# Performance work log

Measured on AMD Instinct MI355X. Metric: run time of the kernel, lower is better.

## Reference

```python
import jax, jax.numpy as jnp
import numpy as np

# dims: batch, nodes, d_node, d_edge, d_attn_hid, heads, d_node_hid, d_edge_hid, layers
B, N, DN, DE, DH, H, DNH, DEH, L = 2, 256, 128, 64, 128, 8, 512, 256, 2
DHH = DH // H  # per-head dim
SCALE = 1.0 / (DH ** 0.5)  # source scales by full d_hid, not per-head dim


def _ln(x, g, b):
    m = jnp.mean(x, -1, keepdims=True)
    v = jnp.mean((x - m) ** 2, -1, keepdims=True)
    return (x - m) * jax.lax.rsqrt(v + 1e-5) * g + b


def _gelu(x):
    return jax.nn.gelu(x, approximate=False)  # torch nn.GELU default = exact erf


def setup_inputs() -> dict:
    key = jax.random.key(0)
    ks = iter(jax.random.split(key, 40))
    def w(shape, scale=0.02):
        return jax.random.normal(next(ks), shape, jnp.float32) * scale
    return {
        "node_features": jax.random.normal(next(ks), (B, N, DN), jnp.float32),
        "edge_features": jax.random.normal(next(ks), (B, N, N, DE), jnp.float32),
        "Wqkv_n": w((L, DN, 3 * DH)),
        "Wqkv_e": w((L, DE, 4 * DH)),
        "Wo": w((L, DH, DN)), "bo": jnp.zeros((L, DN), jnp.float32),
        "Wl0": w((L, DN, DN)), "bl0": jnp.zeros((L, DN), jnp.float32),
        "ln0_g": jnp.ones((L, DN), jnp.float32), "ln0_b": jnp.zeros((L, DN), jnp.float32),
        "Wm1": w((L, DN, DNH)), "Wm2": w((L, DNH, DN)), "bm2": jnp.zeros((L, DN), jnp.float32),
        "ln1_g": jnp.ones((L, DN), jnp.float32), "ln1_b": jnp.zeros((L, DN), jnp.float32),
        "We0": w((L, 2 * DE, DEH)), "be0": jnp.zeros((L, DEH), jnp.float32),
        "Ws": w((L, DN, DEH)), "bs": jnp.zeros((L, DEH), jnp.float32),
        "Wt": w((L, DN, DEH)), "bt": jnp.zeros((L, DEH), jnp.float32),
        "We1": w((L, DEH, DE)), "be1": jnp.zeros((L, DE), jnp.float32),
        "eln0_g": jnp.ones((L, DE), jnp.float32), "eln0_b": jnp.zeros((L, DE), jnp.float32),
        "Wem1": w((L, DE, DEH)), "Wem2": w((L, DEH, DE)), "bem2": jnp.zeros((L, DE), jnp.float32),
        "eln1_g": jnp.ones((L, DE), jnp.float32), "eln1_b": jnp.zeros((L, DE), jnp.float32),
    }


def _forward(node_features, edge_features, Wqkv_n, Wqkv_e, Wo, bo, Wl0, bl0,
             ln0_g, ln0_b, Wm1, Wm2, bm2, ln1_g, ln1_b, We0, be0, Ws, bs, Wt, bt,
             We1, be1, eln0_g, eln0_b, Wem1, Wem2, bem2, eln1_g, eln1_b):
    x, e = node_features, edge_features
    for l in range(L):
        # --- RTAttention (modulate_v=True, eval mode) ---
        qkv_n = (x @ Wqkv_n[l]).reshape(B, N, H, 3 * DHH).transpose(0, 2, 1, 3)  # b h n 3d
        qn, kn, vn = jnp.split(qkv_n, 3, axis=-1)
        qkv_e = (e @ Wqkv_e[l]).reshape(B, N, N, H, 4 * DHH).transpose(0, 3, 1, 2, 4)  # b h i j 4d
        eq, ek, ev, em = jnp.split(qkv_e, 4, axis=-1)
        q = qn[:, :, :, None, :] + eq            # b h i j d
        k = kn[:, :, None, :, :] + ek            # b h i j d
        v = vn[:, :, None, :, :] * em + ev       # modulated values
        dots = SCALE * jnp.einsum('bhijd,bhijd->bhij', q, k)
        attn = jax.nn.softmax(dots, axis=-1)
        out = jnp.einsum('bhij,bhijd->bhid', attn, v)
        out = out.transpose(0, 2, 1, 3).reshape(B, N, DH)
        attn_out = out @ Wo[l] + bo[l]
        # --- node updates: ln(x + lin0(attn)); ln(x + mlp(x)) ---
        x = _ln(x + (attn_out @ Wl0[l] + bl0[l]), ln0_g[l], ln0_b[l])
        x = _ln(x + (_gelu(x @ Wm1[l]) @ Wm2[l] + bm2[l]), ln1_g[l], ln1_b[l])
        # --- edge updates (EdgeLayer) ---
        src = (x @ Ws[l] + bs[l])[:, :, None, :]   # broadcast over target j
        tgt = (x @ Wt[l] + bt[l])[:, None, :, :]   # broadcast over source i
        ecat = jnp.concatenate([e, e.transpose(0, 2, 1, 3)], axis=-1)  # [e_ij, e_ji]
        h = _gelu(ecat @ We0[l] + be0[l] + src + tgt)
        e = _ln(e + (h @ We1[l] + be1[l]), eln0_g[l], eln0_b[l])
        e = _ln(e + (_gelu(e @ Wem1[l]) @ Wem2[l] + bem2[l]), eln1_g[l], eln1_b[l])
    return x, e


def reference(node_features, edge_features, Wqkv_n, Wqkv_e, Wo, bo, Wl0, bl0,
              ln0_g, ln0_b, Wm1, Wm2, bm2, ln1_g, ln1_b, We0, be0, Ws, bs, Wt, bt,
              We1, be1, eln0_g, eln0_b, Wem1, Wem2, bem2, eln1_g, eln1_b):
    return _forward(node_features, edge_features, Wqkv_n, Wqkv_e, Wo, bo, Wl0, bl0,
                    ln0_g, ln0_b, Wm1, Wm2, bm2, ln1_g, ln1_b, We0, be0, Ws, bs, Wt, bt,
                    We1, be1, eln0_g, eln0_b, Wem1, Wem2, bem2, eln1_g, eln1_b)
```

## Files before the change

### kernel.cpp

```cpp
#include <hip/hip_runtime.h>
#include <hip/hip_bf16.h>
#include <stdint.h>

#define BB 2
#define NN 256
#define DN 128
#define DE 64
#define DH 128
#define NH 8
#define DHH 16
#define DNH 512
#define DEH 256
#define NL 2
#define SCALE_ATT 0.08838834764831845f

typedef __hip_bfloat16 bf16;
typedef __attribute__((ext_vector_type(8))) short short8;
typedef __attribute__((ext_vector_type(4))) float f32x4;

__device__ __forceinline__ float gelu_f(float x) {
  return 0.5f * x * (1.0f + erff(x * 0.70710678118654752f));
}
__device__ __forceinline__ float gelu_t(float x) {
  float m2u = x * fmaf(x * x, -0.07135481627f, -1.59576912161f);
  float e = __expf(m2u);
  return x * __builtin_amdgcn_rcpf(1.f + e);
}

__device__ __forceinline__ float wave_sum(float v) {
#pragma unroll
  for (int o = 32; o > 0; o >>= 1) v += __shfl_xor(v, o, 64);
  return v;
}

__device__ __forceinline__ short f2bf(float f) {
  union { float f; uint32_t u; } v{f};
  uint32_t r = (v.u + 0x7FFFu + ((v.u >> 16) & 1u)) >> 16;
  return (short)r;
}
__device__ __forceinline__ float bf2f(short s) {
  union { uint32_t u; float f; } v;
  v.u = ((uint32_t)(uint16_t)s) << 16;
  return v.f;
}

__global__ void k_detect(const uint32_t* g8, const uint32_t* g13, int* flag) {
  if (threadIdx.x == 0 && blockIdx.x == 0) {
    uint32_t a = g8[0], b = g13[0];
    *flag = (a == 0x3F803F80u || b == 0x3F803F80u) ? 1 : 0;
  }
}

struct CastArgs {
  const void* src[30];
  float* dst[30];
  int n[30];
  const int* flag;
};

__global__ __launch_bounds__(256) void k_cast_all(CastArgs a) {
  int ti = blockIdx.y;
  float* d = a.dst[ti];
  int n = a.n[ti];
  int stride = gridDim.x * blockDim.x;
  if (*a.flag) {
    const bf16* s = (const bf16*)a.src[ti];
    for (int i = blockIdx.x * blockDim.x + threadIdx.x; i < n; i += stride)
      d[i] = __bfloat162float(s[i]);
  } else {
    const float* s = (const float*)a.src[ti];
    for (int i = blockIdx.x * blockDim.x + threadIdx.x; i < n; i += stride)
      d[i] = s[i];
  }
}

__global__ __launch_bounds__(256) void k_cast_e(const void* __restrict__ src,
                                                short* __restrict__ dst,
                                                const int* __restrict__ flag) {
  const int n8 = BB * NN * NN * DE / 8;
  int stride = gridDim.x * blockDim.x;
  if (*flag) {
    const uint4* s = (const uint4*)src;
    uint4* d = (uint4*)dst;
    for (int i = blockIdx.x * blockDim.x + threadIdx.x; i < n8; i += stride) d[i] = s[i];
  } else {
    const float4* s = (const float4*)src;
    for (int i = blockIdx.x * blockDim.x + threadIdx.x; i < n8; i += stride) {
      float4 a = s[2 * i], b = s[2 * i + 1];
      short* o = dst + 8 * i;
      o[0] = f2bf(a.x); o[1] = f2bf(a.y); o[2] = f2bf(a.z); o[3] = f2bf(a.w);
      o[4] = f2bf(b.x); o[5] = f2bf(b.y); o[6] = f2bf(b.z); o[7] = f2bf(b.w);
    }
  }
}

__global__ __launch_bounds__(256) void k_cast_out(const float* __restrict__ x,
                                                  const short* __restrict__ e,
                                                  void* __restrict__ out_v,
                                                  const int* __restrict__ flag) {
  const int nx = BB * NN * DN;
  const int total = nx + BB * NN * NN * DE;
  int stride = gridDim.x * blockDim.x;
  if (*flag) {
    short* out = (short*)out_v;
    for (int i = blockIdx.x * blockDim.x + threadIdx.x; i < total; i += stride)
      out[i] = (i < nx) ? f2bf(x[i]) : e[i - nx];
  } else {
    float* out = (float*)out_v;
    for (int i = blockIdx.x * blockDim.x + threadIdx.x; i < total; i += stride)
      out[i] = (i < nx) ? x[i] : bf2f(e[i - nx]);
  }
}

struct WtJob { const float* src; short* dst; int K; int N; };
struct WtArgs { WtJob job[10]; };
__global__ __launch_bounds__(256) void k_wtrans_all(WtArgs a) {
  WtJob j = a.job[blockIdx.y];
  int total = j.K * j.N;
  int stride = gridDim.x * 256;
  for (int idx = blockIdx.x * 256 + threadIdx.x; idx < total; idx += stride) {
    int k = idx / j.N, n = idx - k * j.N;
    j.dst[n * j.K + k] = f2bf(j.src[idx]);
  }
}

__global__ __launch_bounds__(128) void k_node_qkv(const float* __restrict__ x,
                                                  const float* __restrict__ W,
                                                  float* __restrict__ qkv) {
  int row = blockIdx.x;
  __shared__ float xs[DN];
  int t = threadIdx.x;
  xs[t] = x[row * DN + t];
  __syncthreads();
#pragma unroll
  for (int c0 = 0; c0 < 384; c0 += 128) {
    int c = c0 + t;
    float a = 0.f;
    for (int k = 0; k < DN; ++k) a = fmaf(xs[k], W[k * 384 + c], a);
    qkv[row * 384 + c] = a;
  }
}

__global__ __launch_bounds__(256, 3) void k_attn_fused(
    const short* __restrict__ e, const short* __restrict__ WqeT,
    const float* __restrict__ qkv, float* __restrict__ o_buf) {
  int i = blockIdx.x, b = blockIdx.y;
  __shared__ short est[256 * 72];
  __shared__ float sp[NH * NN];
  __shared__ float qnl[DH];
  int t = threadIdx.x;
  for (int idx = t; idx < 2048; idx += 256) {
    int j = idx >> 3, c8 = (idx & 7) * 8;
    *(short8*)(est + j * 72 + c8) =
        *(const short8*)(e + ((size_t)(b * NN + i) * NN + j) * DE + c8);
  }
  if (t < DH) qnl[t] = qkv[(size_t)(b * NN + i) * 384 + (t >> 4) * 48 + (t & 15)];
  __syncthreads();

  int wv = t >> 6, lane = t & 63, g8 = lane >> 4, lo = lane & 15;

  {
    short8 bq[2][2][2];
#pragma unroll
    for (int hh = 0; hh < 2; ++hh)
#pragma unroll
      for (int p = 0; p < 2; ++p)
#pragma unroll
        for (int ks = 0; ks < 2; ++ks)
          bq[hh][p][ks] = *(const short8*)(
              WqeT + (size_t)(((wv * 2 + hh) * 4 + p) * 16 + lo) * 64 + ks * 32 + g8 * 8);
    for (int mt = 0; mt < 16; ++mt) {
      short8 a0 = *(const short8*)(est + (mt * 16 + lo) * 72 + g8 * 8);
      short8 a1 = *(const short8*)(est + (mt * 16 + lo) * 72 + 32 + g8 * 8);
#pragma unroll
      for (int hh = 0; hh < 2; ++hh) {
        int h = wv * 2 + hh;
        float kn4[4];
#pragma unroll
        for (int r = 0; r < 4; ++r)
          kn4[r] = qkv[(size_t)(b * NN + mt * 16 + g8 * 4 + r) * 384 + h * 48 + 16 + lo];
        f32x4 cq = {0.f, 0.f, 0.f, 0.f}, ck = {0.f, 0.f, 0.f, 0.f};
        cq = __builtin_amdgcn_mfma_f32_16x16x32_bf16(a0, bq[hh][0][0], cq, 0, 0, 0);
        cq = __builtin_amdgcn_mfma_f32_16x16x32_bf16(a1, bq[hh][0][1], cq, 0, 0, 0);
        ck = __builtin_amdgcn_mfma_f32_16x16x32_bf16(a0, bq[hh][1][0], ck, 0, 0, 0);
        ck = __builtin_amdgcn_mfma_f32_16x16x32_bf16(a1, bq[hh][1][1], ck, 0, 0, 0);
        float qv = qnl[h * 16 + lo];
#pragma unroll
        for (int r = 0; r < 4; ++r) {
          int j = mt * 16 + g8 * 4 + r;
          float s = (qv + cq[r]) * (kn4[r] + ck[r]);
#pragma unroll
          for (int off = 1; off < 16; off <<= 1) s += __shfl_xor(s, off, 64);
          if (lo == 0) sp[h * NN + j] = s * SCALE_ATT;
        }
      }
    }
  }
  __syncthreads();

#pragma unroll
  for (int hh = 0; hh < 2; ++hh) {
    int h = wv * 2 + hh;
    float v[4];
#pragma unroll
    for (int q = 0; q < 4; ++q) v[q] = sp[h * NN + lane + 64 * q];
    float m = fmaxf(fmaxf(v[0], v[1]), fmaxf(v[2], v[3]));
#pragma unroll
    for (int o = 32; o > 0; o >>= 1) m = fmaxf(m, __shfl_xor(m, o, 64));
    float l = 0.f;
#pragma unroll
    for (int q = 0; q < 4; ++q) { v[q] = __expf(v[q] - m); l += v[q]; }
    l = wave_sum(l);
    float inv = 1.f / l;
#pragma unroll
    for (int q = 0; q < 4; ++q) sp[h * NN + lane + 64 * q] = v[q] * inv;
  }
  __syncthreads();

  {
    short8 bv[2][2][2];
#pragma unroll
    for (int hh = 0; hh < 2; ++hh)
#pragma unroll
      for (int p = 0; p < 2; ++p)
#pragma unroll
        for (int ks = 0; ks < 2; ++ks)
          bv[hh][p][ks] = *(const short8*)(
              WqeT + (size_t)(((wv * 2 + hh) * 4 + 2 + p) * 16 + lo) * 64 + ks * 32 + g8 * 8);
    float oacc[2] = {0.f, 0.f};
    for (int mt = 0; mt < 16; ++mt) {
      short8 a0 = *(const short8*)(est + (mt * 16 + lo) * 72 + g8 * 8);
      short8 a1 = *(const short8*)(est + (mt * 16 + lo) * 72 + 32 + g8 * 8);
#pragma unroll
      for (int hh = 0; hh < 2; ++hh) {
        int h = wv * 2 + hh;
        float vn4[4];
#pragma unroll
        for (int r = 0; r < 4; ++r)
          vn4[r] = qkv[(size_t)(b * NN + mt * 16 + g8 * 4 + r) * 384 + h * 48 + 32 + lo];
        f32x4 cv = {0.f, 0.f, 0.f, 0.f}, cm = {0.f, 0.f, 0.f, 0.f};
        cv = __builtin_amdgcn_mfma_f32_16x16x32_bf16(a0, bv[hh][0][0], cv, 0, 0, 0);
        cv = __builtin_amdgcn_mfma_f32_16x16x32_bf16(a1, bv[hh][0][1], cv, 0, 0, 0);
        cm = __builtin_amdgcn_mfma_f32_16x16x32_bf16(a0, bv[hh][1][0], cm, 0, 0, 0);
        cm = __builtin_amdgcn_mfma_f32_16x16x32_bf16(a1, bv[hh][1][1], cm, 0, 0, 0);
#pragma unroll
        for (int r = 0; r < 4; ++r) {
          int j = mt * 16 + g8 * 4 + r;
          float vv = fmaf(vn4[r], cm[r], cv[r]);
          oacc[hh] = fmaf(sp[h * NN + j], vv, oacc[hh]);
        }
      }
    }
#pragma unroll
    for (int hh = 0; hh < 2; ++hh) {
      int h = wv * 2 + hh;
      float o = oacc[hh];
      o += __shfl_xor(o, 16, 64);
      o += __shfl_xor(o, 32, 64);
      if (g8 == 0) o_buf[(size_t)(b * NN + i) * DH + h * 16 + lo] = o;
    }
  }
}

__global__ __launch_bounds__(256) void k_node_fused(
    const float* __restrict__ o_buf,
    const float* __restrict__ Wo, const float* __restrict__ bo,
    const float* __restrict__ Wl0, const float* __restrict__ bl0,
    const float* __restrict__ g0, const float* __restrict__ b0n,
    const float* __restrict__ Wm1, const float* __restrict__ Wm2,
    const float* __restrict__ bm2, const float* __restrict__ g1,
    const float* __restrict__ b1n, const float* __restrict__ Ws,
    const float* __restrict__ bs, const float* __restrict__ Wt,
    const float* __restrict__ bt, const float* __restrict__ WqnN,
    float* __restrict__ qkv, float* __restrict__ srcb,
    float* __restrict__ tgtb, float* __restrict__ x) {
  int i = blockIdx.x, b = blockIdx.y;
  int row = b * NN + i;
  __shared__ float orow[DH];
  __shared__ float t1s[DH];
  __shared__ float xs[DN];
  __shared__ float hsb[DNH];
  __shared__ float part[256];
  __shared__ float red[4];
  int t = threadIdx.x;
  int col = t & 127, kh = t >> 7;
  if (t < DH) orow[t] = o_buf[(size_t)row * DH + t];
  __syncthreads();
  {
    float a = 0.f;
    int k0 = kh * 64;
    for (int k = k0; k < k0 + 64; ++k) a = fmaf(orow[k], Wo[k * DN + col], a);
    part[t] = a;
  }
  __syncthreads();
  if (t < DH) t1s[t] = part[t] + part[t + 128] + bo[t];
  __syncthreads();
  {
    float a = 0.f;
    int k0 = kh * 64;
    for (int k = k0; k < k0 + 64; ++k) a = fmaf(t1s[k], Wl0[k * DN + col], a);
    part[t] = a;
  }
  __syncthreads();
  if (t < DN) {
    float y = part[t] + part[t + 128] + bl0[t] + x[(size_t)row * DN + t];
    float s1 = wave_sum(y), s2 = wave_sum(y * y);
    if ((t & 63) == 0) { red[t >> 6] = s1; red[2 + (t >> 6)] = s2; }
    part[t] = y;
  }
  __syncthreads();
  if (t < DN) {
    float y = part[t];
    float mean = (red[0] + red[1]) * (1.f / 128.f);
    float var = (red[2] + red[3]) * (1.f / 128.f) - mean * mean;
    float rr = rsqrtf(var + 1e-5f);
    xs[t] = (y - mean) * rr * g0[t] + b0n[t];
  }
  __syncthreads();
#pragma unroll
  for (int p = 0; p < 2; ++p) {
    int c = t + 256 * p;
    float a = 0.f;
    for (int k = 0; k < DN; ++k) a = fmaf(xs[k], Wm1[k * DNH + c], a);
    hsb[c] = gelu_f(a);
  }
  __syncthreads();
  {
    float a = 0.f;
    int k0 = kh * 256;
    for (int k = k0; k < k0 + 256; ++k) a = fmaf(hsb[k], Wm2[k * DN + col], a);
    part[t] = a;
  }
  __syncthreads();
  if (t < DN) {
    float y = part[t] + part[t + 128] + bm2[t] + xs[t];
    float s1 = wave_sum(y), s2 = wave_sum(y * y);
    if ((t & 63) == 0) { red[t >> 6] = s1; red[2 + (t >> 6)] = s2; }
    part[t] = y;
  }
  __syncthreads();
  if (t < DN) {
    float y = part[t];
    float mean = (red[0] + red[1]) * (1.f / 128.f);
    float var = (red[2] + red[3]) * (1.f / 128.f) - mean * mean;
    float rr = rsqrtf(var + 1e-5f);
    float x2 = (y - mean) * rr * g1[t] + b1n[t];
    x[(size_t)row * DN + t] = x2;
    xs[t] = x2;
  }
  __syncthreads();
  {
    float a = bs[t], cc = bt[t];
    for (int k = 0; k < DN; ++k) {
      float xv = xs[k];
      a = fmaf(xv, Ws[k * DEH + t], a);
      cc = fmaf(xv, Wt[k * DEH + t], cc);
    }
    srcb[(size_t)row * DEH + t] = a;
    tgtb[(size_t)row * DEH + t] = cc;
  }
  if (WqnN) {
#pragma unroll
    for (int p = 0; p < 2; ++p) {
      int c = t + 256 * p;
      if (c < 384) {
        float a = 0.f;
        for (int k = 0; k < DN; ++k) a = fmaf(xs[k], WqnN[k * 384 + c], a);
        qkv[(size_t)row * 384 + c] = a;
      }
    }
  }
}

__global__ __launch_bounds__(256, 3) void k_edge_fused(
    const short* __restrict__ e_in, const short* __restrict__ W0T,
    const float* __restrict__ b0, const short* __restrict__ W1T,
    const float* __restrict__ b1, const float* __restrict__ srcb,
    const float* __restrict__ tgtb, const float* __restrict__ g,
    const float* __restrict__ bb, const short* __restrict__ Wm1T,
    const short* __restrict__ Wm2T, const float* __restrict__ bm2,
    const float* __restrict__ gm, const float* __restrict__ bbm,
    short* __restrict__ e_out) {
  int jt = blockIdx.x, i = blockIdx.y, b = blockIdx.z;
  int j0 = jt * 64;
  __shared__ short hidT[64 * 264];
  int t = threadIdx.x;
  int wv = t >> 6, lane = t & 63, g8 = lane >> 4, lo = lane & 15;
  int nq = wv * 64;
  int m0 = wv * 16;

  {
    float bias_n[4];
#pragma unroll
    for (int nt = 0; nt < 4; ++nt)
      bias_n[nt] = b0[nq + nt * 16 + lo] + srcb[(size_t)(b * NN + i) * DEH + nq + nt * 16 + lo];
    short8 bfr1[4][4];
#pragma unroll
    for (int nt = 0; nt < 4; ++nt)
#pragma unroll
      for (int ks = 0; ks < 4; ++ks)
        bfr1[nt][ks] =
            *(const short8*)(W0T + (size_t)(nq + nt * 16 + lo) * 128 + ks * 32 + g8 * 8);
#pragma unroll
    for (int mt = 0; mt < 4; ++mt) {
      int mrow = mt * 16 + lo;
      float tg[4][4];
#pragma unroll
      for (int nt = 0; nt < 4; ++nt)
#pragma unroll
        for (int r = 0; r < 4; ++r)
          tg[nt][r] = tgtb[((size_t)(b * NN) + j0 + mt * 16 + g8 * 4 + r) * DEH +
                           nq + nt * 16 + lo];
      short8 a[4];
      const short* eA = e_in + ((size_t)(b * NN + i) * NN + j0 + mrow) * DE;
#pragma unroll
      for (int ks = 0; ks < 2; ++ks) a[ks] = *(const short8*)(eA + ks * 32 + g8 * 8);
      const short* eT = e_in + ((size_t)(b * NN + j0 + mrow) * NN + i) * DE;
#pragma unroll
      for (int ks = 0; ks < 2; ++ks) a[2 + ks] = *(const short8*)(eT + ks * 32 + g8 * 8);
      f32x4 acc[4];
#pragma unroll
      for (int nt = 0; nt < 4; ++nt) {
        f32x4 c = {0.f, 0.f, 0.f, 0.f};
#pragma unroll
        for (int ks = 0; ks < 4; ++ks)
          c = __builtin_amdgcn_mfma_f32_16x16x32_bf16(a[ks], bfr1[nt][ks], c, 0, 0, 0);
        acc[nt] = c;
      }
#pragma unroll
      for (int nt = 0; nt < 4; ++nt) {
        int n = nq + nt * 16 + lo;
#pragma unroll
        for (int r = 0; r < 4; ++r) {
          int m = mt * 16 + g8 * 4 + r;
          hidT[m * 264 + n] = f2bf(gelu_t(acc[nt][r] + bias_n[nt] + tg[nt][r]));
        }
      }
    }
  }
  float resv[4][4];
#pragma unroll
  for (int nt = 0; nt < 4; ++nt)
#pragma unroll
    for (int r = 0; r < 4; ++r)
      resv[nt][r] = bf2f(e_in[((size_t)(b * NN + i) * NN + j0 + m0 + g8 * 4 + r) * DE +
                              nt * 16 + lo]);
  __syncthreads();

  float emid[4][4];
  {
    short8 a2[8];
#pragma unroll
    for (int ks = 0; ks < 8; ++ks)
      a2[ks] = *(const short8*)(hidT + (m0 + lo) * 264 + ks * 32 + g8 * 8);
    f32x4 acc2[4];
#pragma unroll
    for (int nt = 0; nt < 4; ++nt) {
      f32x4 c = {0.f, 0.f, 0.f, 0.f};
      const short* bp = W1T + (size_t)(nt * 16 + lo) * 256;
#pragma unroll
      for (int ks = 0; ks < 8; ++ks)
        c = __builtin_amdgcn_mfma_f32_16x16x32_bf16(
            a2[ks], *(const short8*)(bp + ks * 32 + g8 * 8), c, 0, 0, 0);
      acc2[nt] = c;
    }
#pragma unroll
    for (int nt = 0; nt < 4; ++nt) {
      int n = nt * 16 + lo;
      float bb1 = b1[n];
#pragma unroll
      for (int r = 0; r < 4; ++r) emid[nt][r] = acc2[nt][r] + bb1 + resv[nt][r];
    }
#pragma unroll
    for (int r = 0; r < 4; ++r) {
      float s = emid[0][r] + emid[1][r] + emid[2][r] + emid[3][r];
      float q = emid[0][r] * emid[0][r] + emid[1][r] * emid[1][r] +
                emid[2][r] * emid[2][r] + emid[3][r] * emid[3][r];
#pragma unroll
      for (int off = 1; off < 16; off <<= 1) {
        s += __shfl_xor(s, off, 64);
        q += __shfl_xor(q, off, 64);
      }
      float mean = s * (1.f / 64.f);
      float var = q * (1.f / 64.f) - mean * mean;
      float rr = rsqrtf(var + 1e-5f);
      int m = m0 + g8 * 4 + r;
#pragma unroll
      for (int nt = 0; nt < 4; ++nt) {
        int n = nt * 16 + lo;
        float v = (emid[nt][r] - mean) * rr * g[n] + bb[n];
        emid[nt][r] = v;
        hidT[m * 264 + n] = f2bf(v);
      }
    }
  }

  {
    short8 a3[2];
#pragma unroll
    for (int ks = 0; ks < 2; ++ks)
      a3[ks] = *(const short8*)(hidT + (m0 + lo) * 264 + ks * 32 + g8 * 8);
#pragma unroll 4
    for (int nt = 0; nt < 16; ++nt) {
      f32x4 c = {0.f, 0.f, 0.f, 0.f};
      const short* bp = Wm1T + (size_t)(nt * 16 + lo) * 64;
#pragma unroll
      for (int ks = 0; ks < 2; ++ks)
        c = __builtin_amdgcn_mfma_f32_16x16x32_bf16(
            a3[ks], *(const short8*)(bp + ks * 32 + g8 * 8), c, 0, 0, 0);
      int n = nt * 16 + lo;
#pragma unroll
      for (int r = 0; r < 4; ++r)
        hidT[(m0 + g8 * 4 + r) * 264 + n] = f2bf(gelu_t(c[r]));
    }
  }

  {
    short8 a4[8];
#pragma unroll
    for (int ks = 0; ks < 8; ++ks)
      a4[ks] = *(const short8*)(hidT + (m0 + lo) * 264 + ks * 32 + g8 * 8);
    f32x4 acc4[4];
#pragma unroll
    for (int nt = 0; nt < 4; ++nt) {
      f32x4 c = {0.f, 0.f, 0.f, 0.f};
      const short* bp = Wm2T + (size_t)(nt * 16 + lo) * 256;
#pragma unroll
      for (int ks = 0; ks < 8; ++ks)
        c = __builtin_amdgcn_mfma_f32_16x16x32_bf16(
            a4[ks], *(const short8*)(bp + ks * 32 + g8 * 8), c, 0, 0, 0);
      acc4[nt] = c;
    }
    float vals[4][4];
#pragma unroll
    for (int nt = 0; nt < 4; ++nt) {
      int n = nt * 16 + lo;
      float bv = bm2[n];
#pragma unroll
      for (int r = 0; r < 4; ++r) vals[nt][r] = acc4[nt][r] + bv + emid[nt][r];
    }
#pragma unroll
    for (int r = 0; r < 4; ++r) {
      float s = vals[0][r] + vals[1][r] + vals[2][r] + vals[3][r];
      float q = vals[0][r] * vals[0][r] + vals[1][r] * vals[1][r] +
                vals[2][r] * vals[2][r] + vals[3][r] * vals[3][r];
#pragma unroll
      for (int off = 1; off < 16; off <<= 1) {
        s += __shfl_xor(s, off, 64);
        q += __shfl_xor(q, off, 64);
      }
      float mean = s * (1.f / 64.f);
      float var = q * (1.f / 64.f) - mean * mean;
      float rr = rsqrtf(var + 1e-5f);
      int m = m0 + g8 * 4 + r;
#pragma unroll
      for (int nt = 0; nt < 4; ++nt) {
        int n = nt * 16 + lo;
        e_out[((size_t)(b * NN + i) * NN + j0 + m) * DE + n] =
            f2bf((vals[nt][r] - mean) * rr * gm[n] + bbm[n]);
      }
    }
  }
}

extern "C" void kernel_launch(void* const* d_in, const int* in_sizes, int n_in,
                              void* d_out, int out_size, void* d_ws, size_t ws_size,
                              hipStream_t stream) {
  float* ws = (float*)d_ws;
  int* flag = (int*)ws;
  size_t off = 64;
  auto alloc = [&](size_t n) {
    float* p = ws + off;
    off += (n + 63) & ~(size_t)63;
    return p;
  };
  float* x_f = alloc((size_t)BB * NN * DN);
  short* e_a = (short*)alloc((size_t)BB * NN * NN * DE / 2);
  short* e_b = (short*)alloc((size_t)BB * NN * NN * DE / 2);
  float* qkv = alloc((size_t)BB * NN * 384);
  float* o_buf = alloc((size_t)BB * NN * DH);
  float* srcb = alloc((size_t)BB * NN * DEH);
  float* tgtb = alloc((size_t)BB * NN * DEH);
  short* WqeT = (short*)alloc(NL * 512 * 64 / 2);
  short* We0T = (short*)alloc(NL * 256 * 128 / 2);
  short* We1T = (short*)alloc(NL * 64 * 256 / 2);
  short* Wem1T = (short*)alloc(NL * 256 * 64 / 2);
  short* Wem2T = (short*)alloc(NL * 64 * 256 / 2);

  float* wf[30];
  wf[0] = x_f;
  wf[1] = x_f;
  CastArgs ca;
  int ntens = n_in < 30 ? n_in : 30;
  for (int idx = 0; idx < ntens; ++idx) {
    if (idx >= 2) wf[idx] = alloc((size_t)in_sizes[idx]);
    ca.src[idx] = d_in[idx];
    ca.dst[idx] = wf[idx];
    ca.n[idx] = (idx == 1) ? 0 : in_sizes[idx];
  }
  ca.flag = flag;

  k_detect<<<1, 64, 0, stream>>>((const uint32_t*)d_in[8], (const uint32_t*)d_in[13], flag);
  k_cast_all<<<dim3(64, ntens), dim3(256), 0, stream>>>(ca);
  k_cast_e<<<1024, 256, 0, stream>>>(d_in[1], e_a, flag);
  WtArgs wa;
  for (int l = 0; l < NL; ++l) {
    wa.job[l * 5 + 0] = {wf[3] + (size_t)l * DE * 512, WqeT + (size_t)l * 512 * 64, DE, 512};
    wa.job[l * 5 + 1] = {wf[15] + (size_t)l * 128 * 256, We0T + (size_t)l * 256 * 128, 128, 256};
    wa.job[l * 5 + 2] = {wf[21] + (size_t)l * 256 * 64, We1T + (size_t)l * 64 * 256, 256, 64};
    wa.job[l * 5 + 3] = {wf[25] + (size_t)l * 64 * 256, Wem1T + (size_t)l * 256 * 64, 64, 256};
    wa.job[l * 5 + 4] = {wf[26] + (size_t)l * 64 * 256, Wem2T + (size_t)l * 64 * 256, 256, 64};
  }
  k_wtrans_all<<<dim3(64, 10), 256, 0, stream>>>(wa);

  k_node_qkv<<<BB * NN, 128, 0, stream>>>(x_f, wf[2], qkv);

  for (int l = 0; l < NL; ++l) {
    const float* Wo = wf[4] + (size_t)l * DH * DN;
    const float* bo = wf[5] + (size_t)l * DN;
    const float* Wl0 = wf[6] + (size_t)l * DN * DN;
    const float* bl0 = wf[7] + (size_t)l * DN;
    const float* g0 = wf[8] + (size_t)l * DN;
    const float* b0n = wf[9] + (size_t)l * DN;
    const float* Wm1 = wf[10] + (size_t)l * DN * DNH;
    const float* Wm2 = wf[11] + (size_t)l * DNH * DN;
    const float* bm2 = wf[12] + (size_t)l * DN;
    const float* g1 = wf[13] + (size_t)l * DN;
    const float* b1n = wf[14] + (size_t)l * DN;
    const float* be0 = wf[16] + (size_t)l * DEH;
    const float* Wsw = wf[17] + (size_t)l * DN * DEH;
    const float* bsw = wf[18] + (size_t)l * DEH;
    const float* Wtw = wf[19] + (size_t)l * DN * DEH;
    const float* btw = wf[20] + (size_t)l * DEH;
    const float* be1 = wf[22] + (size_t)l * DE;
    const float* eg0 = wf[23] + (size_t)l * DE;
    const float* eb0 = wf[24] + (size_t)l * DE;
    const float* bem2 = wf[27] + (size_t)l * DE;
    const float* eg1 = wf[28] + (size_t)l * DE;
    const float* eb1 = wf[29] + (size_t)l * DE;
    const float* WqnNext = (l + 1 < NL) ? (wf[2] + (size_t)(l + 1) * DN * 3 * DH) : nullptr;

    const short* e_cur = (l == 0) ? e_a : e_b;
    short* e_nxt = (l == 0) ? e_b : e_a;

    k_attn_fused<<<dim3(NN, BB), 256, 0, stream>>>(
        e_cur, WqeT + (size_t)l * 512 * 64, qkv, o_buf);
    k_node_fused<<<dim3(NN, BB), 256, 0, stream>>>(
        o_buf, Wo, bo, Wl0, bl0, g0, b0n, Wm1, Wm2, bm2, g1, b1n,
        Wsw, bsw, Wtw, btw, WqnNext, qkv, srcb, tgtb, x_f);
    k_edge_fused<<<dim3(NN / 64, NN, BB), 256, 0, stream>>>(
        e_cur, We0T + (size_t)l * 256 * 128, be0, We1T + (size_t)l * 64 * 256, be1,
        srcb, tgtb, eg0, eb0,
        Wem1T + (size_t)l * 256 * 64, Wem2T + (size_t)l * 64 * 256, bem2, eg1, eb1,
        e_nxt);
  }
  k_cast_out<<<1024, 256, 0, stream>>>(x_f, e_a, d_out, flag);
}
```

Baseline: 583.1 us.

## Swap MFMA operand order so outputs are row-contiguous per lane

Swaps the A and B operands of every MFMA in the attention and edge kernels, so each lane's four accumulator values now lie along the feature dimension instead of across rows. Loads of k/v/bias/target/residual become 16-byte vector loads and LDS/global stores become 8-byte vector writes instead of scalar strided ones. LayerNorm and softmax-score reductions drop from 4-step 16-lane shuffles to 2-step cross-group shuffles. The risk is in correctness of the transposed indexing, and the output reduction in attention now needs more shuffles.

After: 631.0 us. 1.08x slower.

```diff
diff --git a/kernel.cpp b/kernel.cpp
--- a/kernel.cpp
+++ b/kernel.cpp
@@ -16,6 +16,7 @@
 
 typedef __hip_bfloat16 bf16;
 typedef __attribute__((ext_vector_type(8))) short short8;
+typedef __attribute__((ext_vector_type(4))) short short4v;
 typedef __attribute__((ext_vector_type(4))) float f32x4;
 
 __device__ __forceinline__ float gelu_f(float x) {
@@ -147,14 +148,12 @@
   int i = blockIdx.x, b = blockIdx.y;
   __shared__ short est[256 * 72];
   __shared__ float sp[NH * NN];
-  __shared__ float qnl[DH];
   int t = threadIdx.x;
   for (int idx = t; idx < 2048; idx += 256) {
     int j = idx >> 3, c8 = (idx & 7) * 8;
     *(short8*)(est + j * 72 + c8) =
         *(const short8*)(e + ((size_t)(b * NN + i) * NN + j) * DE + c8);
   }
-  if (t < DH) qnl[t] = qkv[(size_t)(b * NN + i) * 384 + (t >> 4) * 48 + (t & 15)];
   __syncthreads();
 
   int wv = t >> 6, lane = t & 63, g8 = lane >> 4, lo = lane & 15;
@@ -169,30 +168,31 @@
         for (int ks = 0; ks < 2; ++ks)
           bq[hh][p][ks] = *(const short8*)(
               WqeT + (size_t)(((wv * 2 + hh) * 4 + p) * 16 + lo) * 64 + ks * 32 + g8 * 8);
+    f32x4 qv4[2];
+#pragma unroll
+    for (int hh = 0; hh < 2; ++hh)
+      qv4[hh] = *(const f32x4*)(
+          qkv + (size_t)(b * NN + i) * 384 + (wv * 2 + hh) * 48 + g8 * 4);
     for (int mt = 0; mt < 16; ++mt) {
       short8 a0 = *(const short8*)(est + (mt * 16 + lo) * 72 + g8 * 8);
       short8 a1 = *(const short8*)(est + (mt * 16 + lo) * 72 + 32 + g8 * 8);
 #pragma unroll
       for (int hh = 0; hh < 2; ++hh) {
         int h = wv * 2 + hh;
-        float kn4[4];
+        f32x4 kn4 = *(const f32x4*)(
+            qkv + (size_t)(b * NN + mt * 16 + lo) * 384 + h * 48 + 16 + g8 * 4);
+        f32x4 cq = {0.f, 0.f, 0.f, 0.f}, ck = {0.f, 0.f, 0.f, 0.f};
+        cq = __builtin_amdgcn_mfma_f32_16x16x32_bf16(bq[hh][0][0], a0, cq, 0, 0, 0);
+        cq = __builtin_amdgcn_mfma_f32_16x16x32_bf16(bq[hh][0][1], a1, cq, 0, 0, 0);
+        ck = __builtin_amdgcn_mfma_f32_16x16x32_bf16(bq[hh][1][0], a0, ck, 0, 0, 0);
+        ck = __builtin_amdgcn_mfma_f32_16x16x32_bf16(bq[hh][1][1], a1, ck, 0, 0, 0);
+        float s = 0.f;
 #pragma unroll
         for (int r = 0; r < 4; ++r)
-          kn4[r] = qkv[(size_t)(b * NN + mt * 16 + g8 * 4 + r) * 384 + h * 48 + 16 + lo];
-        f32x4 cq = {0.f, 0.f, 0.f, 0.f}, ck = {0.f, 0.f, 0.f, 0.f};
-        cq = __builtin_amdgcn_mfma_f32_16x16x32_bf16(a0, bq[hh][0][0], cq, 0, 0, 0);
-        cq = __builtin_amdgcn_mfma_f32_16x16x32_bf16(a1, bq[hh][0][1], cq, 0, 0, 0);
-        ck = __builtin_amdgcn_mfma_f32_16x16x32_bf16(a0, bq[hh][1][0], ck, 0, 0, 0);
-        ck = __builtin_amdgcn_mfma_f32_16x16x32_bf16(a1, bq[hh][1][1], ck, 0, 0, 0);
-        float qv = qnl[h * 16 + lo];
-#pragma unroll
-        for (int r = 0; r < 4; ++r) {
-          int j = mt * 16 + g8 * 4 + r;
-          float s = (qv + cq[r]) * (kn4[r] + ck[r]);
-#pragma unroll
-          for (int off = 1; off < 16; off <<= 1) s += __shfl_xor(s, off, 64);
-          if (lo == 0) sp[h * NN + j] = s * SCALE_ATT;
-        }
+          s = fmaf(qv4[hh][r] + cq[r], kn4[r] + ck[r], s);
+        s += __shfl_xor(s, 16, 64);
+        s += __shfl_xor(s, 32, 64);
+        if (g8 == 0) sp[h * NN + mt * 16 + lo] = s * SCALE_ATT;
       }
     }
   }
@@ -227,37 +227,39 @@
         for (int ks = 0; ks < 2; ++ks)
           bv[hh][p][ks] = *(const short8*)(
               WqeT + (size_t)(((wv * 2 + hh) * 4 + 2 + p) * 16 + lo) * 64 + ks * 32 + g8 * 8);
-    float oacc[2] = {0.f, 0.f};
+    f32x4 oaccT[2] = {{0.f, 0.f, 0.f, 0.f}, {0.f, 0.f, 0.f, 0.f}};
     for (int mt = 0; mt < 16; ++mt) {
       short8 a0 = *(const short8*)(est + (mt * 16 + lo) * 72 + g8 * 8);
       short8 a1 = *(const short8*)(est + (mt * 16 + lo) * 72 + 32 + g8 * 8);
 #pragma unroll
       for (int hh = 0; hh < 2; ++hh) {
         int h = wv * 2 + hh;
-        float vn4[4];
-#pragma unroll
-        for (int r = 0; r < 4; ++r)
-          vn4[r] = qkv[(size_t)(b * NN + mt * 16 + g8 * 4 + r) * 384 + h * 48 + 32 + lo];
+        f32x4 vn4 = *(const f32x4*)(
+            qkv + (size_t)(b * NN + mt * 16 + lo) * 384 + h * 48 + 32 + g8 * 4);
         f32x4 cv = {0.f, 0.f, 0.f, 0.f}, cm = {0.f, 0.f, 0.f, 0.f};
-        cv = __builtin_amdgcn_mfma_f32_16x16x32_bf16(a0, bv[hh][0][0], cv, 0, 0, 0);
-        cv = __builtin_amdgcn_mfma_f32_16x16x32_bf16(a1, bv[hh][0][1], cv, 0, 0, 0);
-        cm = __builtin_amdgcn_mfma_f32_16x16x32_bf16(a0, bv[hh][1][0], cm, 0, 0, 0);
-        cm = __builtin_amdgcn_mfma_f32_16x16x32_bf16(a1, bv[hh][1][1], cm, 0, 0, 0);
+        cv = __builtin_amdgcn_mfma_f32_16x16x32_bf16(bv[hh][0][0], a0, cv, 0, 0, 0);
+        cv = __builtin_amdgcn_mfma_f32_16x16x32_bf16(bv[hh][0][1], a1, cv, 0, 0, 0);
+        cm = __builtin_amdgcn_mfma_f32_16x16x32_bf16(bv[hh][1][0], a0, cm, 0, 0, 0);
+        cm = __builtin_amdgcn_mfma_f32_16x16x32_bf16(bv[hh][1][1], a1, cm, 0, 0, 0);
+        float p = sp[h * NN + mt * 16 + lo];
 #pragma unroll
         for (int r = 0; r < 4; ++r) {
-          int j = mt * 16 + g8 * 4 + r;
           float vv = fmaf(vn4[r], cm[r], cv[r]);
-          oacc[hh] = fmaf(sp[h * NN + j], vv, oacc[hh]);
+          oaccT[hh][r] = fmaf(p, vv, oaccT[hh][r]);
         }
       }
     }
 #pragma unroll
     for (int hh = 0; hh < 2; ++hh) {
       int h = wv * 2 + hh;
-      float o = oacc[hh];
-      o += __shfl_xor(o, 16, 64);
-      o += __shfl_xor(o, 32, 64);
-      if (g8 == 0) o_buf[(size_t)(b * NN + i) * DH + h * 16 + lo] = o;
+      f32x4 o = oaccT[hh];
+#pragma unroll
+      for (int r = 0; r < 4; ++r) {
+#pragma unroll
+        for (int off = 1; off < 16; off <<= 1) o[r] += __shfl_xor(o[r], off, 64);
+      }
+      if (lo == 0)
+        *(f32x4*)(o_buf + (size_t)(b * NN + i) * DH + h * 16 + g8 * 4) = o;
     }
   }
 }
@@ -390,10 +392,11 @@
   int m0 = wv * 16;
 
   {
-    float bias_n[4];
+    f32x4 bias4[4];
 #pragma unroll
     for (int nt = 0; nt < 4; ++nt)
-      bias_n[nt] = b0[nq + nt * 16 + lo] + srcb[(size_t)(b * NN + i) * DEH + nq + nt * 16 + lo];
+      bias4[nt] = *(const f32x4*)(b0 + nq + nt * 16 + g8 * 4) +
+                  *(const f32x4*)(srcb + (size_t)(b * NN + i) * DEH + nq + nt * 16 + g8 * 4);
     short8 bfr1[4][4];
 #pragma unroll
     for (int nt = 0; nt < 4; ++nt)
@@ -404,13 +407,11 @@
 #pragma unroll
     for (int mt = 0; mt < 4; ++mt) {
       int mrow = mt * 16 + lo;
-      float tg[4][4];
+      f32x4 tgv[4];
 #pragma unroll
       for (int nt = 0; nt < 4; ++nt)
-#pragma unroll
-        for (int r = 0; r < 4; ++r)
-          tg[nt][r] = tgtb[((size_t)(b * NN) + j0 + mt * 16 + g8 * 4 + r) * DEH +
-                           nq + nt * 16 + lo];
+        tgv[nt] = *(const f32x4*)(
+            tgtb + ((size_t)(b * NN) + j0 + mrow) * DEH + nq + nt * 16 + g8 * 4);
       short8 a[4];
       const short* eA = e_in + ((size_t)(b * NN + i) * NN + j0 + mrow) * DE;
 #pragma unroll
@@ -418,42 +419,36 @@
       const short* eT = e_in + ((size_t)(b * NN + j0 + mrow) * NN + i) * DE;
 #pragma unroll
       for (int ks = 0; ks < 2; ++ks) a[2 + ks] = *(const short8*)(eT + ks * 32 + g8 * 8);
-      f32x4 acc[4];
 #pragma unroll
       for (int nt = 0; nt < 4; ++nt) {
         f32x4 c = {0.f, 0.f, 0.f, 0.f};
 #pragma unroll
         for (int ks = 0; ks < 4; ++ks)
-          c = __builtin_amdgcn_mfma_f32_16x16x32_bf16(a[ks], bfr1[nt][ks], c, 0, 0, 0);
-        acc[nt] = c;
-      }
-#pragma unroll
-      for (int nt = 0; nt < 4; ++nt) {
-        int n = nq + nt * 16 + lo;
-#pragma unroll
-        for (int r = 0; r < 4; ++r) {
-          int m = mt * 16 + g8 * 4 + r;
-          hidT[m * 264 + n] = f2bf(gelu_t(acc[nt][r] + bias_n[nt] + tg[nt][r]));
-        }
-      }
-    }
-  }
-  float resv[4][4];
-#pragma unroll
-  for (int nt = 0; nt < 4; ++nt)
-#pragma unroll
-    for (int r = 0; r < 4; ++r)
-      resv[nt][r] = bf2f(e_in[((size_t)(b * NN + i) * NN + j0 + m0 + g8 * 4 + r) * DE +
-                              nt * 16 + lo]);
-  __syncthreads();
-
-  float emid[4][4];
+          c = __builtin_amdgcn_mfma_f32_16x16x32_bf16(bfr1[nt][ks], a[ks], c, 0, 0, 0);
+        short4v w;
+#pragma unroll
+        for (int r = 0; r < 4; ++r)
+          w[r] = f2bf(gelu_t(c[r] + bias4[nt][r] + tgv[nt][r]));
+        *(short4v*)(hidT + mrow * 264 + nq + nt * 16 + g8 * 4) = w;
+      }
+    }
+  }
+  f32x4 resv[4];
+#pragma unroll
+  for (int nt = 0; nt < 4; ++nt) {
+    short4v rv = *(const short4v*)(
+        e_in + ((size_t)(b * NN + i) * NN + j0 + m0 + lo) * DE + nt * 16 + g8 * 4);
+#pragma unroll
+    for (int r = 0; r < 4; ++r) resv[nt][r] = bf2f(rv[r]);
+  }
+  __syncthreads();
+
+  f32x4 emid[4];
   {
     short8 a2[8];
 #pragma unroll
     for (int ks = 0; ks < 8; ++ks)
       a2[ks] = *(const short8*)(hidT + (m0 + lo) * 264 + ks * 32 + g8 * 8);
-    f32x4 acc2[4];
 #pragma unroll
     for (int nt = 0; nt < 4; ++nt) {
       f32x4 c = {0.f, 0.f, 0.f, 0.f};
@@ -461,37 +456,35 @@
 #pragma unroll
       for (int ks = 0; ks < 8; ++ks)
         c = __builtin_amdgcn_mfma_f32_16x16x32_bf16(
-            a2[ks], *(const short8*)(bp + ks * 32 + g8 * 8), c, 0, 0, 0);
-      acc2[nt] = c;
-    }
+            *(const short8*)(bp + ks * 32 + g8 * 8), a2[ks], c, 0, 0, 0);
+      f32x4 b14 = *(const f32x4*)(b1 + nt * 16 + g8 * 4);
+      emid[nt] = c + b14 + resv[nt];
+    }
+    float s = 0.f, q = 0.f;
+#pragma unroll
+    for (int nt = 0; nt < 4; ++nt)
+#pragma unroll
+      for (int r = 0; r < 4; ++r) {
+        s += emid[nt][r];
+        q = fmaf(emid[nt][r], emid[nt][r], q);
+      }
+    s += __shfl_xor(s, 16, 64); s += __shfl_xor(s, 32, 64);
+    q += __shfl_xor(q, 16, 64); q += __shfl_xor(q, 32, 64);
+    float mean = s * (1.f / 64.f);
+    float var = q * (1.f / 64.f) - mean * mean;
+    float rr = rsqrtf(var + 1e-5f);
 #pragma unroll
     for (int nt = 0; nt < 4; ++nt) {
-      int n = nt * 16 + lo;
-      float bb1 = b1[n];
-#pragma unroll
-      for (int r = 0; r < 4; ++r) emid[nt][r] = acc2[nt][r] + bb1 + resv[nt][r];
-    }
-#pragma unroll
-    for (int r = 0; r < 4; ++r) {
-      float s = emid[0][r] + emid[1][r] + emid[2][r] + emid[3][r];
-      float q = emid[0][r] * emid[0][r] + emid[1][r] * emid[1][r] +
-                emid[2][r] * emid[2][r] + emid[3][r] * emid[3][r];
-#pragma unroll
-      for (int off = 1; off < 16; off <<= 1) {
-        s += __shfl_xor(s, off, 64);
-        q += __shfl_xor(q, off, 64);
-      }
-      float mean = s * (1.f / 64.f);
-      float var = q * (1.f / 64.f) - mean * mean;
-      float rr = rsqrtf(var + 1e-5f);
-      int m = m0 + g8 * 4 + r;
-#pragma unroll
-      for (int nt = 0; nt < 4; ++nt) {
-        int n = nt * 16 + lo;
-        float v = (emid[nt][r] - mean) * rr * g[n] + bb[n];
+      f32x4 g4 = *(const f32x4*)(g + nt * 16 + g8 * 4);
+      f32x4 bb4 = *(const f32x4*)(bb + nt * 16 + g8 * 4);
+      short4v w;
+#pragma unroll
+      for (int r = 0; r < 4; ++r) {
+        float v = (emid[nt][r] - mean) * rr * g4[r] + bb4[r];
         emid[nt][r] = v;
-        hidT[m * 264 + n] = f2bf(v);
-      }
+        w[r] = f2bf(v);
+      }
+      *(short4v*)(hidT + (m0 + lo) * 264 + nt * 16 + g8 * 4) = w;
     }
   }
 
@@ -507,11 +500,11 @@
 #pragma unroll
       for (int ks = 0; ks < 2; ++ks)
         c = __builtin_amdgcn_mfma_f32_16x16x32_bf16(
-            a3[ks], *(const short8*)(bp + ks * 32 + g8 * 8), c, 0, 0, 0);
-      int n = nt * 16 + lo;
-#pragma unroll
-      for (int r = 0; r < 4; ++r)
-        hidT[(m0 + g8 * 4 + r) * 264 + n] = f2bf(gelu_t(c[r]));
+            *(const short8*)(bp + ks * 32 + g8 * 8), a3[ks], c, 0, 0, 0);
+      short4v w;
+#pragma unroll
+      for (int r = 0; r < 4; ++r) w[r] = f2bf(gelu_t(c[r]));
+      *(short4v*)(hidT + (m0 + lo) * 264 + nt * 16 + g8 * 4) = w;
     }
   }
 
@@ -520,7 +513,7 @@
 #pragma unroll
     for (int ks = 0; ks < 8; ++ks)
       a4[ks] = *(const short8*)(hidT + (m0 + lo) * 264 + ks * 32 + g8 * 8);
-    f32x4 acc4[4];
+    f32x4 vals[4];
 #pragma unroll
     for (int nt = 0; nt < 4; ++nt) {
       f32x4 c = {0.f, 0.f, 0.f, 0.f};
@@ -528,37 +521,33 @@
 #pragma unroll
       for (int ks = 0; ks < 8; ++ks)
         c = __builtin_amdgcn_mfma_f32_16x16x32_bf16(
-            a4[ks], *(const short8*)(bp + ks * 32 + g8 * 8), c, 0, 0, 0);
-      acc4[nt] = c;
-    }
-    float vals[4][4];
+            *(const short8*)(bp + ks * 32 + g8 * 8), a4[ks], c, 0, 0, 0);
+      f32x4 bv4 = *(const f32x4*)(bm2 + nt * 16 + g8 * 4);
+      vals[nt] = c + bv4 + emid[nt];
+    }
+    float s = 0.f, q = 0.f;
+#pragma unroll
+    for (int nt = 0; nt < 4; ++nt)
+#pragma unroll
+      for (int r = 0; r < 4; ++r) {
+        s += vals[nt][r];
+        q = fmaf(vals[nt][r], vals[nt][r], q);
+      }
+    s += __shfl_xor(s, 16, 64); s += __shfl_xor(s, 32, 64);
+    q += __shfl_xor(q, 16, 64); q += __shfl_xor(q, 32, 64);
+    float mean = s * (1.f / 64.f);
+    float var = q * (1.f / 64.f) - mean * mean;
+    float rr = rsqrtf(var + 1e-5f);
+    short* orow = e_out + ((size_t)(b * NN + i) * NN + j0 + m0 + lo) * DE;
 #pragma unroll
     for (int nt = 0; nt < 4; ++nt) {
-      int n = nt * 16 + lo;
-      float bv = bm2[n];
-#pragma unroll
-      for (int r = 0; r < 4; ++r) vals[nt][r] = acc4[nt][r] + bv + emid[nt][r];
-    }
-#pragma unroll
-    for (int r = 0; r < 4; ++r) {
-      float s = vals[0][r] + vals[1][r] + vals[2][r] + vals[3][r];
-      float q = vals[0][r] * vals[0][r] + vals[1][r] * vals[1][r] +
-                vals[2][r] * vals[2][r] + vals[3][r] * vals[3][r];
-#pragma unroll
-      for (int off = 1; off < 16; off <<= 1) {
-        s += __shfl_xor(s, off, 64);
-        q += __shfl_xor(q, off, 64);
-      }
-      float mean = s * (1.f / 64.f);
-      float var = q * (1.f / 64.f) - mean * mean;
-      float rr = rsqrtf(var + 1e-5f);
-      int m = m0 + g8 * 4 + r;
-#pragma unroll
-      for (int nt = 0; nt < 4; ++nt) {
-        int n = nt * 16 + lo;
-        e_out[((size_t)(b * NN + i) * NN + j0 + m) * DE + n] =
-            f2bf((vals[nt][r] - mean) * rr * gm[n] + bbm[n]);
-      }
+      f32x4 g4 = *(const f32x4*)(gm + nt * 16 + g8 * 4);
+      f32x4 bb4 = *(const f32x4*)(bbm + nt * 16 + g8 * 4);
+      short4v w;
+#pragma unroll
+      for (int r = 0; r < 4; ++r)
+        w[r] = f2bf((vals[nt][r] - mean) * rr * g4[r] + bb4[r]);
+      *(short4v*)(orow + nt * 16 + g8 * 4) = w;
     }
   }
 }
```
